# Kernel optimization log

Measured on AMD Instinct MI355X. Metric: run time of the kernel, lower is better.

Reference implementation:

```python
import jax, jax.numpy as jnp
import numpy as np

B, T, U = 4, 200, 100
ENC_DIM = 512
PRED_DIM = 512
JOINT_DIM = 640
VOCAB = 1024


def setup_inputs() -> dict:
    key = jax.random.key(0)
    k = jax.random.split(key, 5)
    return {
        "enc_out": jax.random.normal(k[0], (B, T, ENC_DIM), dtype=jnp.float32),
        "pred_out": jax.random.normal(k[1], (B, U, PRED_DIM), dtype=jnp.float32),
        "W_enc": jax.random.normal(k[2], (ENC_DIM, JOINT_DIM), dtype=jnp.float32) / np.sqrt(ENC_DIM),
        "b_enc": jnp.zeros((JOINT_DIM,), dtype=jnp.float32),
        "W_pred": jax.random.normal(k[3], (PRED_DIM, JOINT_DIM), dtype=jnp.float32) / np.sqrt(PRED_DIM),
        "W_out": jax.random.normal(k[4], (JOINT_DIM, VOCAB), dtype=jnp.float32) / np.sqrt(JOINT_DIM),
        "b_out": jnp.zeros((VOCAB,), dtype=jnp.float32),
    }


def reference(enc_out, pred_out, W_enc, b_enc, W_pred, W_out, b_out):
    # Project encoder and prediction-net outputs to joint_dim.
    enc = jnp.einsum("bte,ej->btj", enc_out, W_enc) + b_enc      # [B,T,J]
    pred = jnp.einsum("bup,pj->buj", pred_out, W_pred)           # [B,U,J] (no bias)
    # Broadcast add -> tanh -> vocab projection.
    joint = jnp.tanh(enc[:, :, None, :] + pred[:, None, :, :])   # [B,T,U,J]
    logits = jnp.einsum("btuj,jv->btuv", joint, W_out) + b_out   # [B,T,U,V]
    return logits
```

## Files before the change

### kernel.cpp

```cpp
#include <hip/hip_runtime.h>
#include <hip/hip_bf16.h>

#define B_ 4
#define T_ 200
#define U_ 100
#define ENC_DIM 512
#define JDIM 640
#define VOCAB 1024
#define M_TOTAL (B_*T_*U_)

typedef __attribute__((ext_vector_type(8))) short short8;
typedef __attribute__((ext_vector_type(4))) float float4v;
typedef __attribute__((ext_vector_type(4))) unsigned short ushort4v;
typedef __attribute__((ext_vector_type(8))) unsigned short ushort8v;

__device__ __forceinline__ unsigned short f2bf(float x) {
    unsigned u = __builtin_bit_cast(unsigned, x);
    u += 0x7fffu + ((u >> 16) & 1u);
    return (unsigned short)(u >> 16);
}

__device__ __forceinline__ float fast_tanh(float x) {
    return 1.0f - 2.0f / (__expf(2.0f * x) + 1.0f);
}

__device__ __forceinline__ void gload_lds16(const void* g, void* l) {
    __builtin_amdgcn_global_load_lds(
        (const __attribute__((address_space(1))) unsigned int*)g,
        (__attribute__((address_space(3))) unsigned int*)l, 16, 0, 0);
}

#define PBM 16
#define PBN 64
#define PBK 32

__global__ __launch_bounds__(256)
void proj_tiled(const float* __restrict__ X, const float* __restrict__ W,
                const float* __restrict__ bias, float* __restrict__ Y, int M) {
    __shared__ float Xs[PBM][PBK + 4];
    __shared__ float Ws[PBK][PBN + 4];
    const int tid = threadIdx.x;
    const int row0 = blockIdx.x * PBM;
    const int col0 = blockIdx.y * PBN;

    const int xr = tid >> 3;
    const int xk = (tid & 7) * 4;
    const int wk = tid >> 4;
    const int wn = (tid & 15) * 4;

    const int ty = tid >> 4;
    const int tx = tid & 15;

    int xrow = row0 + xr; if (xrow >= M) xrow = M - 1;

    float4v acc = {0.f, 0.f, 0.f, 0.f};

    for (int k0 = 0; k0 < ENC_DIM; k0 += PBK) {
        if (tid < 128)
            *(float4v*)&Xs[xr][xk] = *(const float4v*)(X + (size_t)xrow * ENC_DIM + k0 + xk);
        #pragma unroll
        for (int i = 0; i < 2; ++i)
            *(float4v*)&Ws[wk + i*16][wn] =
                *(const float4v*)(W + (size_t)(k0 + wk + i*16) * JDIM + col0 + wn);
        __syncthreads();
        #pragma unroll
        for (int k = 0; k < PBK; ++k) {
            float a = Xs[ty][k];
            float4v w = *(const float4v*)&Ws[k][tx * 4];
            acc += w * a;
        }
        __syncthreads();
    }

    float4v bb = {0.f,0.f,0.f,0.f};
    if (bias) bb = *(const float4v*)(bias + col0 + tx * 4);
    int r0 = row0 + ty;
    if (r0 < M) *(float4v*)(Y + (size_t)r0 * JDIM + col0 + tx*4) = acc + bb;
}

__global__ __launch_bounds__(256)
void transpose_cast(const float* __restrict__ W, unsigned short* __restrict__ Wt) {
    __shared__ float tile[32][33];
    const int bk = blockIdx.x;
    const int bn = blockIdx.y;
    const int tx = threadIdx.x;
    const int ty = threadIdx.y;
    #pragma unroll
    for (int i = 0; i < 32; i += 8)
        tile[ty + i][tx] = W[(bk * 32 + ty + i) * VOCAB + bn * 32 + tx];
    __syncthreads();
    #pragma unroll
    for (int i = 0; i < 32; i += 8)
        Wt[(bn * 32 + ty + i) * JDIM + bk * 32 + tx] = f2bf(tile[tx][ty + i]);
}

__global__ __launch_bounds__(256)
void joint_tanh(const float* __restrict__ encp, const float* __restrict__ predp,
                unsigned short* __restrict__ jbuf, int m0, int mcount) {
    int idx = blockIdx.x * 256 + threadIdx.x;
    if (idx >= mcount * (JDIM / 8)) return;
    int m  = idx / (JDIM / 8);
    int c8 = (idx - m * (JDIM / 8)) * 8;
    int mg = m0 + m;
    int b   = mg / (T_ * U_);
    int rem = mg - b * (T_ * U_);
    int t   = rem / U_;
    int u   = rem - t * U_;
    const float* eRow = encp  + (size_t)(b * T_ + t) * JDIM + c8;
    const float* pRow = predp + (size_t)(b * U_ + u) * JDIM + c8;
    float4v e0 = *(const float4v*)(eRow);
    float4v e1 = *(const float4v*)(eRow + 4);
    float4v p0 = *(const float4v*)(pRow);
    float4v p1 = *(const float4v*)(pRow + 4);
    ushort8v v;
    v.s0 = f2bf(fast_tanh(e0.x + p0.x));
    v.s1 = f2bf(fast_tanh(e0.y + p0.y));
    v.s2 = f2bf(fast_tanh(e0.z + p0.z));
    v.s3 = f2bf(fast_tanh(e0.w + p0.w));
    v.s4 = f2bf(fast_tanh(e1.x + p1.x));
    v.s5 = f2bf(fast_tanh(e1.y + p1.y));
    v.s6 = f2bf(fast_tanh(e1.z + p1.z));
    v.s7 = f2bf(fast_tanh(e1.w + p1.w));
    *(ushort8v*)(jbuf + (size_t)m * JDIM + c8) = v;
}

#define GBM 128
#define GBN 128
#define GBK 128
#define NBN (VOCAB / GBN)

__global__ __launch_bounds__(256, 2)
void gemm_joint(const unsigned short* __restrict__ A,
                const unsigned short* __restrict__ Wt,
                const float* __restrict__ bout,
                float* __restrict__ out)
{
    __shared__ __align__(16) unsigned short As[GBM * GBK];
    __shared__ __align__(16) unsigned short Bs[GBN * GBK];

    const int tid = threadIdx.x;

    const int cpx = gridDim.x >> 3;
    const int bid = blockIdx.x;
    const int swz = (bid & 7) * cpx + (bid >> 3);
    const int bm = swz >> 3;
    const int bn = swz & (NBN - 1);

    const int srow = tid >> 4;
    const int schunk = tid & 15;
    const int scolSwz = (schunk ^ (srow & 7)) * 8;
    const unsigned short* aBase = A  + (size_t)(bm * GBM + srow) * JDIM + scolSwz;
    const unsigned short* bBase = Wt + (size_t)(bn * GBN + srow) * JDIM + scolSwz;
    unsigned short* asDst = &As[srow * GBK + schunk * 8];
    unsigned short* bsDst = &Bs[srow * GBK + schunk * 8];

    const int wave = tid >> 6, lane = tid & 63;
    const int wm = (wave >> 1) * 64, wn = (wave & 1) * 64;
    const int lm = lane & 15, quad = lane >> 4;
    const int rx = lm & 7;

    float4v acc[4][4];
    #pragma unroll
    for (int i = 0; i < 4; ++i)
        #pragma unroll
        for (int j = 0; j < 4; ++j)
            acc[i][j] = (float4v){0.f, 0.f, 0.f, 0.f};

    for (int k0 = 0; k0 < JDIM; k0 += GBK) {
        #pragma unroll
        for (int i = 0; i < 8; ++i) {
            gload_lds16(aBase + (size_t)(i * 16) * JDIM + k0, asDst + i * 16 * GBK);
            gload_lds16(bBase + (size_t)(i * 16) * JDIM + k0, bsDst + i * 16 * GBK);
        }
        __syncthreads();

        #pragma unroll
        for (int kk = 0; kk < GBK; kk += 32) {
            const int cp = (((kk >> 3) + quad) ^ rx) * 8;
            short8 a[4], b[4];
            #pragma unroll
            for (int i = 0; i < 4; ++i)
                a[i] = *(const short8*)(&As[(wm + i * 16 + lm) * GBK + cp]);
            #pragma unroll
            for (int j = 0; j < 4; ++j)
                b[j] = *(const short8*)(&Bs[(wn + j * 16 + lm) * GBK + cp]);
            #pragma unroll
            for (int i = 0; i < 4; ++i)
                #pragma unroll
                for (int j = 0; j < 4; ++j)
                    acc[i][j] = __builtin_amdgcn_mfma_f32_16x16x32_bf16(a[i], b[j], acc[i][j], 0, 0, 0);
        }
        __syncthreads();
    }

    #pragma unroll
    for (int j = 0; j < 4; ++j) {
        int ng = bn * GBN + wn + j * 16 + lm;
        float bias = bout[ng];
        #pragma unroll
        for (int i = 0; i < 4; ++i) {
            int mg0 = bm * GBM + wm + i * 16 + quad * 4;
            #pragma unroll
            for (int r = 0; r < 4; ++r)
                __builtin_nontemporal_store(acc[i][j][r] + bias,
                                            out + (size_t)(mg0 + r) * VOCAB + ng);
        }
    }
}

#define BM 128
#define BN 128
#define BK 64
#define LDST 72

__global__ __launch_bounds__(256, 2)
void joint_gemm_fused(const float* __restrict__ encp, const float* __restrict__ predp,
                      const unsigned short* __restrict__ Wt, const float* __restrict__ bout,
                      float* __restrict__ out)
{
    __shared__ __align__(16) unsigned short As[BM * LDST];
    __shared__ __align__(16) unsigned short Bs[BN * LDST];
    const int tid = threadIdx.x;
    const int bm = blockIdx.x, bn = blockIdx.y;
    const int rbase = tid >> 4;
    const int c4 = (tid & 15) * 4;
    int encOff[8], predOff[8];
    #pragma unroll
    for (int i = 0; i < 8; ++i) {
        int mg  = bm * BM + i * 16 + rbase;
        int b   = mg / (T_ * U_);
        int rem = mg - b * (T_ * U_);
        int t   = rem / U_;
        int u   = rem - t * U_;
        encOff[i]  = (b * T_ + t) * JDIM + c4;
        predOff[i] = (b * U_ + u) * JDIM + c4;
    }
    const int nrow = tid >> 3;
    const int bk8  = (tid & 7) * 8;
    const size_t wtBase = (size_t)(bn * BN) * JDIM;
    const int wave = tid >> 6, lane = tid & 63;
    const int wm = (wave >> 1) * 64, wn = (wave & 1) * 64;
    const int lm = lane & 15, quad = lane >> 4;

    float4v acc[4][4];
    #pragma unroll
    for (int i = 0; i < 4; ++i)
        #pragma unroll
        for (int j = 0; j < 4; ++j)
            acc[i][j] = (float4v){0.f, 0.f, 0.f, 0.f};

    for (int k0 = 0; k0 < JDIM; k0 += BK) {
        #pragma unroll
        for (int i = 0; i < 8; ++i) {
            int row = i * 16 + rbase;
            float4v e4 = *(const float4v*)(encp + encOff[i] + k0);
            float4v p4 = *(const float4v*)(predp + predOff[i] + k0);
            ushort4v v;
            v.x = f2bf(fast_tanh(e4.x + p4.x));
            v.y = f2bf(fast_tanh(e4.y + p4.y));
            v.z = f2bf(fast_tanh(e4.z + p4.z));
            v.w = f2bf(fast_tanh(e4.w + p4.w));
            *(ushort4v*)(&As[row * LDST + c4]) = v;
        }
        #pragma unroll
        for (int i = 0; i < 4; ++i) {
            int n = i * 32 + nrow;
            float4v w = *(const float4v*)((const float*)(Wt + wtBase + (size_t)n * JDIM + k0 + bk8));
            *(float4v*)(&Bs[n * LDST + bk8]) = w;
        }
        __syncthreads();
        #pragma unroll
        for (int kk = 0; kk < BK; kk += 32) {
            short8 a[4], b[4];
            #pragma unroll
            for (int i = 0; i < 4; ++i)
                a[i] = *(const short8*)(&As[(wm + i * 16 + lm) * LDST + kk + quad * 8]);
            #pragma unroll
            for (int j = 0; j < 4; ++j)
                b[j] = *(const short8*)(&Bs[(wn + j * 16 + lm) * LDST + kk + quad * 8]);
            #pragma unroll
            for (int i = 0; i < 4; ++i)
                #pragma unroll
                for (int j = 0; j < 4; ++j)
                    acc[i][j] = __builtin_amdgcn_mfma_f32_16x16x32_bf16(a[i], b[j], acc[i][j], 0, 0, 0);
        }
        __syncthreads();
    }
    #pragma unroll
    for (int j = 0; j < 4; ++j) {
        int ng = bn * BN + wn + j * 16 + lm;
        float bias = bout[ng];
        #pragma unroll
        for (int i = 0; i < 4; ++i) {
            int mg0 = bm * BM + wm + i * 16 + quad * 4;
            #pragma unroll
            for (int r = 0; r < 4; ++r)
                out[(size_t)(mg0 + r) * VOCAB + ng] = acc[i][j][r] + bias;
        }
    }
}

extern "C" void kernel_launch(void* const* d_in, const int* in_sizes, int n_in,
                              void* d_out, int out_size, void* d_ws, size_t ws_size,
                              hipStream_t stream) {
    const float* enc_out  = (const float*)d_in[0];
    const float* pred_out = (const float*)d_in[1];
    const float* W_enc    = (const float*)d_in[2];
    const float* b_enc    = (const float*)d_in[3];
    const float* W_pred   = (const float*)d_in[4];
    const float* W_out    = (const float*)d_in[5];
    const float* b_out    = (const float*)d_in[6];
    float* out = (float*)d_out;

    float* encp  = (float*)d_ws;
    float* predp = encp + 800 * JDIM;
    unsigned short* Wt = (unsigned short*)(predp + 400 * JDIM);
    unsigned short* jbuf = Wt + (size_t)VOCAB * JDIM;

    const size_t fixedBytes = (800 * JDIM + 400 * JDIM) * sizeof(float)
                            + (size_t)VOCAB * JDIM * sizeof(unsigned short);

    proj_tiled<<<dim3(800 / PBM, 10), 256, 0, stream>>>(enc_out, W_enc, b_enc, encp, 800);
    proj_tiled<<<dim3(400 / PBM, 10), 256, 0, stream>>>(pred_out, W_pred, nullptr, predp, 400);
    transpose_cast<<<dim3(20, 32), dim3(32, 8), 0, stream>>>(W_out, Wt);

    size_t avail = ws_size > fixedBytes ? ws_size - fixedBytes : 0;
    long mcMax = (long)(avail / (JDIM * sizeof(unsigned short)));
    mcMax = (mcMax / 128) * 128;
    if (mcMax > M_TOTAL) mcMax = M_TOTAL;

    if (mcMax >= 8192) {
        for (int m0 = 0; m0 < M_TOTAL; m0 += (int)mcMax) {
            int mc = M_TOTAL - m0 < mcMax ? M_TOTAL - m0 : (int)mcMax;
            int nThreads = mc * (JDIM / 8);
            joint_tanh<<<(nThreads + 255) / 256, 256, 0, stream>>>(encp, predp, jbuf, m0, mc);
            gemm_joint<<<dim3((mc / GBM) * NBN), 256, 0, stream>>>(jbuf, Wt, b_out,
                                                                   out + (size_t)m0 * VOCAB);
        }
    } else {
        joint_gemm_fused<<<dim3(M_TOTAL / BM, VOCAB / BN), 256, 0, stream>>>(encp, predp, Wt, b_out, out);
    }
}
```

Baseline: 484.4 us.

## Double-buffer the joint GEMM K loop and merge prep kernels into one launch

```diff
diff --git a/kernel.cpp b/kernel.cpp
--- a/kernel.cpp
+++ b/kernel.cpp
@@ -30,68 +30,107 @@
         (__attribute__((address_space(3))) unsigned int*)l, 16, 0, 0);
 }
 
-#define PBM 16
-#define PBN 64
-#define PBK 32
+#define PJ_BM 32
+#define PJ_BN 128
+#define PJ_BK 32
+#define NCB   (JDIM / PJ_BN)
+#define ENC_RB 25
+#define PRED_RB 13
+#define ENC_BLOCKS  (ENC_RB * NCB)
+#define PRED_BLOCKS (PRED_RB * NCB)
+#define TC_BLOCKS   (20 * 32)
+#define PREP_BLOCKS (ENC_BLOCKS + PRED_BLOCKS + TC_BLOCKS)
+
+#define XS_LD 36
+#define WS_LD 132
 
 __global__ __launch_bounds__(256)
-void proj_tiled(const float* __restrict__ X, const float* __restrict__ W,
-                const float* __restrict__ bias, float* __restrict__ Y, int M) {
-    __shared__ float Xs[PBM][PBK + 4];
-    __shared__ float Ws[PBK][PBN + 4];
+void prep(const float* __restrict__ enc_out, const float* __restrict__ pred_out,
+          const float* __restrict__ W_enc, const float* __restrict__ b_enc,
+          const float* __restrict__ W_pred, const float* __restrict__ W_out,
+          float* __restrict__ encp, float* __restrict__ predp,
+          unsigned short* __restrict__ Wt)
+{
+    __shared__ float smem[PJ_BM * XS_LD + PJ_BK * WS_LD];
+    const int bid = blockIdx.x;
     const int tid = threadIdx.x;
-    const int row0 = blockIdx.x * PBM;
-    const int col0 = blockIdx.y * PBN;
-
-    const int xr = tid >> 3;
-    const int xk = (tid & 7) * 4;
-    const int wk = tid >> 4;
-    const int wn = (tid & 15) * 4;
-
-    const int ty = tid >> 4;
-    const int tx = tid & 15;
-
-    int xrow = row0 + xr; if (xrow >= M) xrow = M - 1;
-
-    float4v acc = {0.f, 0.f, 0.f, 0.f};
-
-    for (int k0 = 0; k0 < ENC_DIM; k0 += PBK) {
-        if (tid < 128)
-            *(float4v*)&Xs[xr][xk] = *(const float4v*)(X + (size_t)xrow * ENC_DIM + k0 + xk);
-        #pragma unroll
-        for (int i = 0; i < 2; ++i)
-            *(float4v*)&Ws[wk + i*16][wn] =
-                *(const float4v*)(W + (size_t)(k0 + wk + i*16) * JDIM + col0 + wn);
+
+    if (bid < ENC_BLOCKS + PRED_BLOCKS) {
+        const float* X; const float* W; const float* bias; float* Y; int M; int lb;
+        if (bid < ENC_BLOCKS) {
+            X = enc_out; W = W_enc; bias = b_enc; Y = encp; M = 800; lb = bid;
+        } else {
+            X = pred_out; W = W_pred; bias = nullptr; Y = predp; M = 400; lb = bid - ENC_BLOCKS;
+        }
+        const int row0 = (lb / NCB) * PJ_BM;
+        const int col0 = (lb % NCB) * PJ_BN;
+
+        float* Xs = smem;
+        float* Ws = smem + PJ_BM * XS_LD;
+
+        const int xr = tid >> 3;
+        const int xk = (tid & 7) * 4;
+        const int wrow = tid >> 5;
+        const int wcol = (tid & 31) * 4;
+        const int ty = tid >> 4;
+        const int tx = tid & 15;
+
+        int xrow = row0 + xr; if (xrow >= M) xrow = M - 1;
+
+        float4v acc00 = {0,0,0,0}, acc01 = {0,0,0,0};
+        float4v acc10 = {0,0,0,0}, acc11 = {0,0,0,0};
+
+        for (int k0 = 0; k0 < ENC_DIM; k0 += PJ_BK) {
+            *(float4v*)&Xs[xr * XS_LD + xk] =
+                *(const float4v*)(X + (size_t)xrow * ENC_DIM + k0 + xk);
+            #pragma unroll
+            for (int r = 0; r < 4; ++r)
+                *(float4v*)&Ws[(wrow + 8*r) * WS_LD + wcol] =
+                    *(const float4v*)(W + (size_t)(k0 + wrow + 8*r) * JDIM + col0 + wcol);
+            __syncthreads();
+            #pragma unroll
+            for (int k4 = 0; k4 < PJ_BK / 4; ++k4) {
+                float4v a0 = *(const float4v*)&Xs[ty * XS_LD + k4*4];
+                float4v a1 = *(const float4v*)&Xs[(ty + 16) * XS_LD + k4*4];
+                #pragma unroll
+                for (int q = 0; q < 4; ++q) {
+                    float4v w0 = *(const float4v*)&Ws[(k4*4 + q) * WS_LD + tx*4];
+                    float4v w1 = *(const float4v*)&Ws[(k4*4 + q) * WS_LD + tx*4 + 64];
+                    float a0q = a0[q], a1q = a1[q];
+                    acc00 += w0 * a0q;  acc01 += w1 * a0q;
+                    acc10 += w0 * a1q;  acc11 += w1 * a1q;
+                }
+            }
+            __syncthreads();
+        }
+
+        const int c0 = col0 + tx*4, c1 = c0 + 64;
+        float4v bb0 = {0,0,0,0}, bb1 = {0,0,0,0};
+        if (bias) { bb0 = *(const float4v*)(bias + c0); bb1 = *(const float4v*)(bias + c1); }
+        int r0 = row0 + ty, r1 = row0 + ty + 16;
+        if (r0 < M) {
+            *(float4v*)(Y + (size_t)r0 * JDIM + c0) = acc00 + bb0;
+            *(float4v*)(Y + (size_t)r0 * JDIM + c1) = acc01 + bb1;
+        }
+        if (r1 < M) {
+            *(float4v*)(Y + (size_t)r1 * JDIM + c0) = acc10 + bb0;
+            *(float4v*)(Y + (size_t)r1 * JDIM + c1) = acc11 + bb1;
+        }
+    } else {
+        float (*tile)[33] = (float(*)[33])smem;
+        const int local = bid - (ENC_BLOCKS + PRED_BLOCKS);
+        const int bk = local % 20;
+        const int bn = local / 20;
+        const int tx = tid & 31;
+        const int ty = tid >> 5;
+        #pragma unroll
+        for (int i = 0; i < 32; i += 8)
+            tile[ty + i][tx] = W_out[(size_t)(bk * 32 + ty + i) * VOCAB + bn * 32 + tx];
         __syncthreads();
         #pragma unroll
-        for (int k = 0; k < PBK; ++k) {
-            float a = Xs[ty][k];
-            float4v w = *(const float4v*)&Ws[k][tx * 4];
-            acc += w * a;
-        }
-        __syncthreads();
-    }
-
-    float4v bb = {0.f,0.f,0.f,0.f};
-    if (bias) bb = *(const float4v*)(bias + col0 + tx * 4);
-    int r0 = row0 + ty;
-    if (r0 < M) *(float4v*)(Y + (size_t)r0 * JDIM + col0 + tx*4) = acc + bb;
-}
-
-__global__ __launch_bounds__(256)
-void transpose_cast(const float* __restrict__ W, unsigned short* __restrict__ Wt) {
-    __shared__ float tile[32][33];
-    const int bk = blockIdx.x;
-    const int bn = blockIdx.y;
-    const int tx = threadIdx.x;
-    const int ty = threadIdx.y;
-    #pragma unroll
-    for (int i = 0; i < 32; i += 8)
-        tile[ty + i][tx] = W[(bk * 32 + ty + i) * VOCAB + bn * 32 + tx];
-    __syncthreads();
-    #pragma unroll
-    for (int i = 0; i < 32; i += 8)
-        Wt[(bn * 32 + ty + i) * JDIM + bk * 32 + tx] = f2bf(tile[tx][ty + i]);
+        for (int i = 0; i < 32; i += 8)
+            Wt[(size_t)(bn * 32 + ty + i) * JDIM + bk * 32 + tx] = f2bf(tile[tx][ty + i]);
+    }
 }
 
 __global__ __launch_bounds__(256)
@@ -126,8 +165,9 @@
 
 #define GBM 128
 #define GBN 128
-#define GBK 128
+#define GBK 64
 #define NBN (VOCAB / GBN)
+#define NTILES (JDIM / GBK)
 
 __global__ __launch_bounds__(256, 2)
 void gemm_joint(const unsigned short* __restrict__ A,
@@ -135,8 +175,8 @@
                 const float* __restrict__ bout,
                 float* __restrict__ out)
 {
-    __shared__ __align__(16) unsigned short As[GBM * GBK];
-    __shared__ __align__(16) unsigned short Bs[GBN * GBK];
+    __shared__ __align__(16) unsigned short As[2][GBM * GBK];
+    __shared__ __align__(16) unsigned short Bs[2][GBN * GBK];
 
     const int tid = threadIdx.x;
 
@@ -146,13 +186,12 @@
     const int bm = swz >> 3;
     const int bn = swz & (NBN - 1);
 
-    const int srow = tid >> 4;
-    const int schunk = tid & 15;
+    const int srow = tid >> 3;
+    const int schunk = tid & 7;
     const int scolSwz = (schunk ^ (srow & 7)) * 8;
     const unsigned short* aBase = A  + (size_t)(bm * GBM + srow) * JDIM + scolSwz;
     const unsigned short* bBase = Wt + (size_t)(bn * GBN + srow) * JDIM + scolSwz;
-    unsigned short* asDst = &As[srow * GBK + schunk * 8];
-    unsigned short* bsDst = &Bs[srow * GBK + schunk * 8];
+    const int ldsOff = tid * 8;
 
     const int wave = tid >> 6, lane = tid & 63;
     const int wm = (wave >> 1) * 64, wn = (wave & 1) * 64;
@@ -166,32 +205,51 @@
         for (int j = 0; j < 4; ++j)
             acc[i][j] = (float4v){0.f, 0.f, 0.f, 0.f};
 
-    for (int k0 = 0; k0 < JDIM; k0 += GBK) {
-        #pragma unroll
-        for (int i = 0; i < 8; ++i) {
-            gload_lds16(aBase + (size_t)(i * 16) * JDIM + k0, asDst + i * 16 * GBK);
-            gload_lds16(bBase + (size_t)(i * 16) * JDIM + k0, bsDst + i * 16 * GBK);
-        }
-        __syncthreads();
-
-        #pragma unroll
-        for (int kk = 0; kk < GBK; kk += 32) {
-            const int cp = (((kk >> 3) + quad) ^ rx) * 8;
-            short8 a[4], b[4];
-            #pragma unroll
-            for (int i = 0; i < 4; ++i)
-                a[i] = *(const short8*)(&As[(wm + i * 16 + lm) * GBK + cp]);
-            #pragma unroll
-            for (int j = 0; j < 4; ++j)
-                b[j] = *(const short8*)(&Bs[(wn + j * 16 + lm) * GBK + cp]);
-            #pragma unroll
-            for (int i = 0; i < 4; ++i)
-                #pragma unroll
-                for (int j = 0; j < 4; ++j)
-                    acc[i][j] = __builtin_amdgcn_mfma_f32_16x16x32_bf16(a[i], b[j], acc[i][j], 0, 0, 0);
-        }
-        __syncthreads();
-    }
+#define STAGE(buf, k0)                                                          \
+    {                                                                           \
+        _Pragma("unroll")                                                       \
+        for (int r = 0; r < 4; ++r) {                                           \
+            gload_lds16(aBase + (size_t)(r * 32) * JDIM + (k0), &As[buf][ldsOff + r * 2048]); \
+            gload_lds16(bBase + (size_t)(r * 32) * JDIM + (k0), &Bs[buf][ldsOff + r * 2048]); \
+        }                                                                       \
+    }
+
+#define COMPUTE(buf)                                                            \
+    {                                                                           \
+        _Pragma("unroll")                                                       \
+        for (int kk = 0; kk < GBK; kk += 32) {                                  \
+            const int cp = (((kk >> 3) + quad) ^ rx) * 8;                       \
+            short8 a[4], b[4];                                                  \
+            _Pragma("unroll")                                                   \
+            for (int i = 0; i < 4; ++i)                                         \
+                a[i] = *(const short8*)(&As[buf][(wm + i * 16 + lm) * GBK + cp]); \
+            _Pragma("unroll")                                                   \
+            for (int j = 0; j < 4; ++j)                                         \
+                b[j] = *(const short8*)(&Bs[buf][(wn + j * 16 + lm) * GBK + cp]); \
+            _Pragma("unroll")                                                   \
+            for (int i = 0; i < 4; ++i)                                         \
+                _Pragma("unroll")                                               \
+                for (int j = 0; j < 4; ++j)                                     \
+                    acc[i][j] = __builtin_amdgcn_mfma_f32_16x16x32_bf16(a[i], b[j], acc[i][j], 0, 0, 0); \
+        }                                                                       \
+    }
+
+    STAGE(0, 0);
+    asm volatile("s_waitcnt vmcnt(0)" ::: "memory");
+    __builtin_amdgcn_s_barrier();
+
+    int cur = 0;
+    for (int t = 0; t < NTILES - 1; ++t) {
+        STAGE(cur ^ 1, (t + 1) * GBK);
+        COMPUTE(cur);
+        asm volatile("s_waitcnt vmcnt(0)" ::: "memory");
+        __builtin_amdgcn_s_barrier();
+        cur ^= 1;
+    }
+    COMPUTE(cur);
+
+#undef STAGE
+#undef COMPUTE
 
     #pragma unroll
     for (int j = 0; j < 4; ++j) {
@@ -320,9 +378,8 @@
     const size_t fixedBytes = (800 * JDIM + 400 * JDIM) * sizeof(float)
                             + (size_t)VOCAB * JDIM * sizeof(unsigned short);
 
-    proj_tiled<<<dim3(800 / PBM, 10), 256, 0, stream>>>(enc_out, W_enc, b_enc, encp, 800);
-    proj_tiled<<<dim3(400 / PBM, 10), 256, 0, stream>>>(pred_out, W_pred, nullptr, predp, 400);
-    transpose_cast<<<dim3(20, 32), dim3(32, 8), 0, stream>>>(W_out, Wt);
+    prep<<<dim3(PREP_BLOCKS), 256, 0, stream>>>(enc_out, pred_out, W_enc, b_enc,
+                                                W_pred, W_out, encp, predp, Wt);
 
     size_t avail = ws_size > fixedBytes ? ws_size - fixedBytes : 0;
     long mcMax = (long)(avail / (JDIM * sizeof(unsigned short)));
```

After: 464.3 us. 1.04x faster.
